# Kernel tuning notes

Hardware: AMD Instinct MI355X
Metric: run time of the kernel (lower is better)

Reference implementation:

```python
import jax, jax.numpy as jnp
import numpy as np

N_HEADS = 16
EMBED_DIM = 2048
BATCH, SEQ = 2, 2048


def setup_inputs() -> dict:
    key = jax.random.key(0)
    k1, k2, k3, k4, k5 = jax.random.split(key, 5)
    s_in = 1.0 / np.sqrt(EMBED_DIM)
    return {
        "x": jax.random.normal(k1, (BATCH, SEQ, EMBED_DIM), dtype=jnp.float32),
        "w_in": jax.random.normal(k2, (3 * EMBED_DIM, EMBED_DIM), dtype=jnp.float32) * s_in,
        "b_in": jax.random.normal(k3, (3 * EMBED_DIM,), dtype=jnp.float32) * 0.02,
        "w_out": jax.random.normal(k4, (EMBED_DIM, EMBED_DIM), dtype=jnp.float32) * s_in,
        "b_out": jax.random.normal(k5, (EMBED_DIM,), dtype=jnp.float32) * 0.02,
        "causal_mask": 1,
    }


def reference(x, w_in, b_in, w_out, b_out, causal_mask):
    b, l, e = x.shape
    h, d = N_HEADS, e // N_HEADS
    qkv = x @ w_in.T + b_in                      # [b, l, 3e]
    q, k, v = jnp.split(qkv, 3, axis=-1)
    # b l (h d) -> b h l d
    q = q.reshape(b, l, h, d).transpose(0, 2, 1, 3)
    k = k.reshape(b, l, h, d).transpose(0, 2, 1, 3)
    v = v.reshape(b, l, h, d).transpose(0, 2, 1, 3)
    scores = jnp.einsum("bhqd,bhkd->bhqk", q, k) / jnp.sqrt(jnp.float32(d))
    if causal_mask:
        tri = jnp.triu(jnp.ones((l, l), dtype=bool), k=1)  # True above diagonal
        scores = jnp.where(tri, -jnp.inf, scores)
    attn = jax.nn.softmax(scores, axis=-1)
    out = jnp.einsum("bhqk,bhkd->bhqd", attn, v)  # [b, h, l, d]
    out = out.transpose(0, 2, 1, 3).reshape(b, l, e)
    return out @ w_out.T + b_out
```

## Files before the change

kernel.cpp:

```cpp
#include <hip/hip_runtime.h>
#include <hip/hip_bf16.h>
#include <math.h>

typedef __attribute__((ext_vector_type(4))) float floatx4;
typedef __attribute__((ext_vector_type(16))) float floatx16;
typedef __attribute__((ext_vector_type(8))) __bf16 bf16x8;

__device__ __forceinline__ unsigned short f2bf(float f) {
    union { float f; unsigned int u; } v; v.f = f;
    unsigned int u = v.u;
    u += 0x7FFFu + ((u >> 16) & 1u);
    return (unsigned short)(u >> 16);
}

__device__ __forceinline__ unsigned int pkbf(float a, float b) {
    return (unsigned int)f2bf(a) | ((unsigned int)f2bf(b) << 16);
}

__device__ __forceinline__ void gl_lds16(const void* g, void* l) {
    __builtin_amdgcn_global_load_lds(
        (const __attribute__((address_space(1))) void*)g,
        (__attribute__((address_space(3))) void*)l, 16, 0, 0);
}

__global__ void cast_f32_bf16(const float* __restrict__ in,
                              unsigned short* __restrict__ out, int n) {
    int i = (blockIdx.x * blockDim.x + threadIdx.x) * 4;
    if (i + 4 <= n) {
        float4 f = *(const float4*)(in + i);
        ushort4 o;
        o.x = f2bf(f.x); o.y = f2bf(f.y); o.z = f2bf(f.z); o.w = f2bf(f.w);
        *(ushort4*)(out + i) = o;
    }
}

#define BM 128
#define BN 128
#define BK 32

template<int MODE>
__global__ __launch_bounds__(256) void gemm_nt(
    const unsigned short* __restrict__ A,
    const unsigned short* __restrict__ B,
    const float* __restrict__ bias,
    float* __restrict__ Cf,
    unsigned short* __restrict__ q_ws,
    unsigned short* __restrict__ k_ws,
    unsigned short* __restrict__ vT_ws,
    int M, int N, int K)
{
    __shared__ unsigned short Asm[BM][BK];
    __shared__ unsigned short Bsm[BN][BK];

    const int bx = blockIdx.x, by = blockIdx.y;
    const int m0 = by * BM, n0 = bx * BN;
    const int tid = threadIdx.x;
    const int lane = tid & 63, wid = tid >> 6;
    const int quad = lane >> 4, li = lane & 15;
    const int wy = wid >> 1, wx = wid & 1;

    const int lrow = lane >> 2;
    const int lcol = (lane & 3) * 8;

    floatx4 acc[4][4] = {};

    const int kTiles = K / BK;
    for (int kt = 0; kt < kTiles; ++kt) {
        const int k0 = kt * BK;
        #pragma unroll
        for (int c = 0; c < 2; ++c) {
            const int cidx = wid * 2 + c;
            const int row = cidx * 16 + lrow;
            gl_lds16(A + (size_t)(m0 + row) * K + k0 + lcol,
                     &Asm[0][0] + cidx * 512);
            gl_lds16(B + (size_t)(n0 + row) * K + k0 + lcol,
                     &Bsm[0][0] + cidx * 512);
        }
        __syncthreads();

        bf16x8 af[4], bfr[4];
        #pragma unroll
        for (int t = 0; t < 4; ++t) {
            af[t]  = *(const bf16x8*)(&Asm[wy * 64 + t * 16 + li][quad * 8]);
            bfr[t] = *(const bf16x8*)(&Bsm[wx * 64 + t * 16 + li][quad * 8]);
        }
        #pragma unroll
        for (int i = 0; i < 4; ++i)
            #pragma unroll
            for (int j = 0; j < 4; ++j)
                acc[i][j] = __builtin_amdgcn_mfma_f32_16x16x32_bf16(
                    af[i], bfr[j], acc[i][j], 0, 0, 0);
        __syncthreads();
    }

    if (MODE == 0) {
        #pragma unroll
        for (int i = 0; i < 4; ++i)
            #pragma unroll
            for (int j = 0; j < 4; ++j) {
                int col = wx * 64 + j * 16 + li;
                float bv = bias[n0 + col];
                #pragma unroll
                for (int r = 0; r < 4; ++r) {
                    int row = wy * 64 + i * 16 + quad * 4 + r;
                    Cf[(size_t)(m0 + row) * N + n0 + col] = acc[i][j][r] + bv;
                }
            }
    } else {
        const int which = bx >> 4;
        const int h = bx & 15;
        const int b = by >> 4;
        const int lbase = (by & 15) * BM;
        const size_t bh = (size_t)(b * 16 + h);
        #pragma unroll
        for (int i = 0; i < 4; ++i)
            #pragma unroll
            for (int j = 0; j < 4; ++j) {
                int col = wx * 64 + j * 16 + li;
                float bv = bias[n0 + col];
                #pragma unroll
                for (int r = 0; r < 4; ++r) {
                    int row = wy * 64 + i * 16 + quad * 4 + r;
                    int l = lbase + row;
                    unsigned short ob = f2bf(acc[i][j][r] + bv);
                    if (which == 0)      q_ws[(bh * 2048 + l) * 128 + col] = ob;
                    else if (which == 1) k_ws[(bh * 2048 + l) * 128 + col] = ob;
                    else                 vT_ws[(bh * 128 + col) * 2048 + l] = ob;
                }
            }
    }
}

#define AP 8
__global__ __launch_bounds__(256, 1) void attn_kernel(
    const unsigned short* __restrict__ q_ws,
    const unsigned short* __restrict__ k_ws,
    const unsigned short* __restrict__ vT_ws,
    unsigned short* __restrict__ aout,
    const int* __restrict__ causal_ptr)
{
    __shared__ unsigned short Ksm[128][128 + AP];
    __shared__ unsigned short Vsm[128][128 + AP];

    const int ord = blockIdx.x;
    int qt, bhid;
    if (ord < 256) { qt = ord >> 5;              bhid = ord & 31; }
    else           { qt = 15 - ((ord - 256) >> 5); bhid = ord & 31; }
    const int b = bhid >> 4, h = bhid & 15;

    const int tid = threadIdx.x;
    const int lane = tid & 63, w = tid >> 6;
    const int lq = lane & 31;
    const int half = lane >> 5;
    const size_t bh = (size_t)(b * 16 + h);
    const unsigned short* Qp = q_ws + bh * 2048 * 128;
    const unsigned short* Kp = k_ws + bh * 2048 * 128;
    const unsigned short* Vp = vT_ws + bh * 128 * 2048;
    const int causal = causal_ptr[0];
    const float scale = 0.08838834764831845f;

    const int qg = qt * 128 + w * 32 + lq;
    bf16x8 qf[8];
    #pragma unroll
    for (int s = 0; s < 8; ++s)
        qf[s] = *(const bf16x8*)(Qp + (size_t)qg * 128 + s * 16 + half * 8);

    floatx16 O[4] = {};
    float m_i = -INFINITY, l_i = 0.f;

    const int myEnd = causal ? qt : 15;
    for (int kt = 0; kt <= myEnd; ++kt) {
        #pragma unroll
        for (int c = 0; c < 8; ++c) {
            int chunk = c * 256 + tid;
            int row = chunk >> 4;
            int cc  = (chunk & 15) * 8;
            *(uint4*)(&Ksm[row][cc]) =
                *(const uint4*)(Kp + (size_t)(kt * 128 + row) * 128 + cc);
            *(uint4*)(&Vsm[row][cc]) =
                *(const uint4*)(Vp + (size_t)row * 2048 + kt * 128 + cc);
        }
        __syncthreads();

        const bool diag = causal && (kt == qt);
        #pragma unroll 1
        for (int ch = 0; ch < 2; ++ch) {
            floatx16 S[2] = {};
            #pragma unroll
            for (int c2 = 0; c2 < 2; ++c2) {
                const int ct = ch * 2 + c2;
                #pragma unroll
                for (int s = 0; s < 8; ++s) {
                    bf16x8 kf = *(const bf16x8*)(&Ksm[ct * 32 + lq][s * 16 + half * 8]);
                    S[c2] = __builtin_amdgcn_mfma_f32_32x32x16_bf16(kf, qf[s], S[c2], 0, 0, 0);
                }
            }

            float mx = -INFINITY;
            #pragma unroll
            for (int c2 = 0; c2 < 2; ++c2)
                #pragma unroll
                for (int r = 0; r < 16; ++r) {
                    float sv = S[c2][r] * scale;
                    if (diag) {
                        int key = 32 * (ch * 2 + c2) + (r & 3) + 8 * (r >> 2) + 4 * half;
                        if (kt * 128 + key > qg) sv = -INFINITY;
                    }
                    S[c2][r] = sv;
                    mx = fmaxf(mx, sv);
                }
            mx = fmaxf(mx, __shfl_xor(mx, 32, 64));
            float m_new = fmaxf(m_i, mx);
            float m_use = (m_new == -INFINITY) ? 0.f : m_new;
            float alpha = __expf(m_i - m_use);

            float rs = 0.f;
            #pragma unroll
            for (int c2 = 0; c2 < 2; ++c2)
                #pragma unroll
                for (int r = 0; r < 16; ++r) {
                    float p = __expf(S[c2][r] - m_use);
                    S[c2][r] = p;
                    rs += p;
                }
            rs += __shfl_xor(rs, 32, 64);
            l_i = l_i * alpha + rs;
            m_i = (m_new == -INFINITY) ? m_i : m_new;
            #pragma unroll
            for (int dt = 0; dt < 4; ++dt)
                #pragma unroll
                for (int r = 0; r < 16; ++r)
                    O[dt][r] *= alpha;

            bf16x8 pfr[4];
            #pragma unroll
            for (int c2 = 0; c2 < 2; ++c2)
                #pragma unroll
                for (int h2 = 0; h2 < 2; ++h2) {
                    int base = 8 * h2;
                    unsigned int pk0 = pkbf(S[c2][base + 0], S[c2][base + 1]);
                    unsigned int pk1 = pkbf(S[c2][base + 2], S[c2][base + 3]);
                    unsigned int pk2 = pkbf(S[c2][base + 4], S[c2][base + 5]);
                    unsigned int pk3 = pkbf(S[c2][base + 6], S[c2][base + 7]);
                    unsigned int x0 = __shfl_xor((int)pk0, 32, 64);
                    unsigned int x1 = __shfl_xor((int)pk1, 32, 64);
                    unsigned int x2 = __shfl_xor((int)pk2, 32, 64);
                    unsigned int x3 = __shfl_xor((int)pk3, 32, 64);
                    union { unsigned int u[4]; bf16x8 v; } fr;
                    fr.u[0] = half ? x2 : pk0;
                    fr.u[1] = half ? x3 : pk1;
                    fr.u[2] = half ? pk2 : x0;
                    fr.u[3] = half ? pk3 : x1;
                    pfr[c2 * 2 + h2] = fr.v;
                }

            #pragma unroll
            for (int dt = 0; dt < 4; ++dt)
                #pragma unroll
                for (int p = 0; p < 4; ++p) {
                    int s = ch * 4 + p;
                    bf16x8 vf = *(const bf16x8*)(&Vsm[dt * 32 + lq][s * 16 + half * 8]);
                    O[dt] = __builtin_amdgcn_mfma_f32_32x32x16_bf16(vf, pfr[p], O[dt], 0, 0, 0);
                }
        }
        __syncthreads();
    }

    const float invl = 1.0f / l_i;
    #pragma unroll
    for (int dt = 0; dt < 4; ++dt)
        #pragma unroll
        for (int g = 0; g < 4; ++g) {
            int dbase = dt * 32 + g * 8 + half * 4;
            ushort4 o4;
            o4.x = f2bf(O[dt][g * 4 + 0] * invl);
            o4.y = f2bf(O[dt][g * 4 + 1] * invl);
            o4.z = f2bf(O[dt][g * 4 + 2] * invl);
            o4.w = f2bf(O[dt][g * 4 + 3] * invl);
            *(ushort4*)(&Ksm[w * 32 + lq][dbase]) = o4;
        }
    __syncthreads();
    #pragma unroll
    for (int c = 0; c < 8; ++c) {
        int chunk = c * 256 + tid;
        int row = chunk >> 4;
        int dc = (chunk & 15) * 8;
        uint4 v = *(const uint4*)(&Ksm[row][dc]);
        *(uint4*)(aout + ((size_t)b * 2048 + qt * 128 + row) * 2048 + h * 128 + dc) = v;
    }
}

extern "C" void kernel_launch(void* const* d_in, const int* in_sizes, int n_in,
                              void* d_out, int out_size, void* d_ws, size_t ws_size,
                              hipStream_t stream) {
    const float* x     = (const float*)d_in[0];
    const float* w_in  = (const float*)d_in[1];
    const float* b_in  = (const float*)d_in[2];
    const float* w_out = (const float*)d_in[3];
    const float* b_out = (const float*)d_in[4];
    const int* causal  = (const int*)d_in[5];

    char* ws = (char*)d_ws;
    unsigned short* xb    = (unsigned short*)ws; ws += (size_t)4096 * 2048 * 2;
    unsigned short* wb    = (unsigned short*)ws; ws += (size_t)6144 * 2048 * 2;
    unsigned short* wob   = (unsigned short*)ws; ws += (size_t)2048 * 2048 * 2;
    unsigned short* q_ws  = (unsigned short*)ws; ws += (size_t)32 * 2048 * 128 * 2;
    unsigned short* k_ws  = (unsigned short*)ws; ws += (size_t)32 * 2048 * 128 * 2;
    unsigned short* vT_ws = (unsigned short*)ws; ws += (size_t)32 * 2048 * 128 * 2;
    unsigned short* aout  = (unsigned short*)ws; ws += (size_t)4096 * 2048 * 2;

    cast_f32_bf16<<<8192, 256, 0, stream>>>(x, xb, 4096 * 2048);
    cast_f32_bf16<<<12288, 256, 0, stream>>>(w_in, wb, 6144 * 2048);
    cast_f32_bf16<<<4096, 256, 0, stream>>>(w_out, wob, 2048 * 2048);

    gemm_nt<1><<<dim3(48, 32), 256, 0, stream>>>(
        xb, wb, b_in, nullptr, q_ws, k_ws, vT_ws, 4096, 6144, 2048);

    attn_kernel<<<512, 256, 0, stream>>>(
        q_ws, k_ws, vT_ws, aout, causal);

    gemm_nt<0><<<dim3(16, 32), 256, 0, stream>>>(
        aout, wob, b_out, (float*)d_out, nullptr, nullptr, nullptr,
        4096, 2048, 2048);
}
```

Before: 446.2 us.

## Double GEMM K-tile with XOR-swizzled LDS and remap attention blocks per XCD

The GEMM K tile grows from 32 to 64, which halves the number of barrier pairs per output tile. Global-to-LDS loads now use an XOR swizzle on 16-byte chunks so the MFMA fragment reads avoid LDS bank conflicts. The attention grid is remapped so each XCD processes four fixed batch-heads, alternating short and long causal query tiles, with the aim of better L2 locality for K/V and better load balance. The cost is double the LDS per GEMM block, which may reduce occupancy.

```diff
diff --git a/kernel.cpp b/kernel.cpp
--- a/kernel.cpp
+++ b/kernel.cpp
@@ -36,7 +36,7 @@
 
 #define BM 128
 #define BN 128
-#define BK 32
+#define BK 64
 
 template<int MODE>
 __global__ __launch_bounds__(256) void gemm_nt(
@@ -59,8 +59,8 @@
     const int quad = lane >> 4, li = lane & 15;
     const int wy = wid >> 1, wx = wid & 1;
 
-    const int lrow = lane >> 2;
-    const int lcol = (lane & 3) * 8;
+    const int lrow8 = lane >> 3;
+    const int lswz  = ((lane & 7) ^ lrow8) * 8;
 
     floatx4 acc[4][4] = {};
 
@@ -68,28 +68,33 @@
     for (int kt = 0; kt < kTiles; ++kt) {
         const int k0 = kt * BK;
         #pragma unroll
-        for (int c = 0; c < 2; ++c) {
-            const int cidx = wid * 2 + c;
-            const int row = cidx * 16 + lrow;
-            gl_lds16(A + (size_t)(m0 + row) * K + k0 + lcol,
-                     &Asm[0][0] + cidx * 512);
-            gl_lds16(B + (size_t)(n0 + row) * K + k0 + lcol,
-                     &Bsm[0][0] + cidx * 512);
+        for (int c = 0; c < 4; ++c) {
+            const int inst = wid * 4 + c;
+            const int row = inst * 8 + lrow8;
+            gl_lds16(A + (size_t)(m0 + row) * K + k0 + lswz,
+                     (char*)&Asm[0][0] + inst * 1024);
+            gl_lds16(B + (size_t)(n0 + row) * K + k0 + lswz,
+                     (char*)&Bsm[0][0] + inst * 1024);
         }
         __syncthreads();
 
-        bf16x8 af[4], bfr[4];
-        #pragma unroll
-        for (int t = 0; t < 4; ++t) {
-            af[t]  = *(const bf16x8*)(&Asm[wy * 64 + t * 16 + li][quad * 8]);
-            bfr[t] = *(const bf16x8*)(&Bsm[wx * 64 + t * 16 + li][quad * 8]);
-        }
-        #pragma unroll
-        for (int i = 0; i < 4; ++i)
-            #pragma unroll
-            for (int j = 0; j < 4; ++j)
-                acc[i][j] = __builtin_amdgcn_mfma_f32_16x16x32_bf16(
-                    af[i], bfr[j], acc[i][j], 0, 0, 0);
+        #pragma unroll
+        for (int s2 = 0; s2 < 2; ++s2) {
+            bf16x8 af[4], bfr[4];
+            #pragma unroll
+            for (int t = 0; t < 4; ++t) {
+                const int col8 = s2 * 4 + quad;
+                const int cswz = (col8 ^ (li & 7)) * 8;
+                af[t]  = *(const bf16x8*)(&Asm[wy * 64 + t * 16 + li][cswz]);
+                bfr[t] = *(const bf16x8*)(&Bsm[wx * 64 + t * 16 + li][cswz]);
+            }
+            #pragma unroll
+            for (int i = 0; i < 4; ++i)
+                #pragma unroll
+                for (int j = 0; j < 4; ++j)
+                    acc[i][j] = __builtin_amdgcn_mfma_f32_16x16x32_bf16(
+                        af[i], bfr[j], acc[i][j], 0, 0, 0);
+        }
         __syncthreads();
     }
 
@@ -143,16 +148,19 @@
     __shared__ unsigned short Vsm[128][128 + AP];
 
     const int ord = blockIdx.x;
-    int qt, bhid;
-    if (ord < 256) { qt = ord >> 5;              bhid = ord & 31; }
-    else           { qt = 15 - ((ord - 256) >> 5); bhid = ord & 31; }
+    const int xcd = ord & 7;
+    const int slot = ord >> 3;
+    const int bhl = slot & 3;
+    const int sq = slot >> 2;
+    const int qt = (sq & 1) ? (15 - (sq >> 1)) : (sq >> 1);
+    const int bhid = xcd * 4 + bhl;
     const int b = bhid >> 4, h = bhid & 15;
 
     const int tid = threadIdx.x;
     const int lane = tid & 63, w = tid >> 6;
     const int lq = lane & 31;
     const int half = lane >> 5;
-    const size_t bh = (size_t)(b * 16 + h);
+    const size_t bh = (size_t)bhid;
     const unsigned short* Qp = q_ws + bh * 2048 * 128;
     const unsigned short* Kp = k_ws + bh * 2048 * 128;
     const unsigned short* Vp = vT_ws + bh * 128 * 2048;
```

Result: no change. 443.0 us (-0.7%).
